# Optimization experiments

Hardware: AMD Instinct MI355X
Metric: run time of the kernel (lower is better)

## Reference

```python
import math
import jax, jax.numpy as jnp
import numpy as np

LN_EPS = 1e-5
SIG_DOMAIN = 5.0


def _layer_norm(x, gamma, beta):
    mu = jnp.mean(x, axis=-1, keepdims=True)
    var = jnp.var(x, axis=-1, keepdims=True)
    return (x - mu) / jnp.sqrt(var + LN_EPS) * gamma + beta


def setup_inputs() -> dict:
    key = jax.random.key(0)
    k0, k1, k2, k3 = jax.random.split(key, 4)
    B, H, S, D = 4, 16, 1024, 256   # batch, c_heads, seq, input_dim
    A, O = 128, 256                 # attention_dim, output_dim
    x = jax.random.normal(k0, (B, H, S, D), dtype=jnp.float32)
    # torch.rand -> uniform [0,1)
    W_query = jax.random.uniform(k1, (H, A, D), dtype=jnp.float32)
    W_key = jax.random.uniform(k2, (H, A, D), dtype=jnp.float32)
    W_value = jax.random.uniform(k3, (H, O, D), dtype=jnp.float32)
    gamma = jnp.ones((D,), dtype=jnp.float32)
    beta = jnp.zeros((D,), dtype=jnp.float32)
    return {"x": x, "W_query": W_query, "W_key": W_key, "W_value": W_value,
            "gamma": gamma, "beta": beta}


def reference(x, W_query, W_key, W_value, gamma, beta):
    scale = math.sqrt(x.shape[-1])  # sqrt(input_dim)
    xn = _layer_norm(x, gamma, beta)                       # [B,H,S,D]
    q = jnp.einsum('bhsd,had->bhsa', xn, W_query)          # [B,H,S,A]
    k = jnp.einsum('bhsd,had->bhsa', xn, W_key)            # [B,H,S,A]
    v = jnp.einsum('bhsd,hod->bhso', xn, W_value)          # [B,H,S,O]
    scores = jnp.einsum('bhsa,bhta->bhst', q, k) / scale   # [B,H,S,S]
    # overtaking-sigmoid-tuned normalization
    s_max = jnp.max(scores, axis=-1, keepdims=True)
    s_min = jnp.min(scores, axis=-1, keepdims=True)
    s_norm = (scores - s_min) / (s_max - s_min)
    softmax_sel = 1.0 - jax.nn.sigmoid(
        (1.0 - jnp.max(s_norm, axis=-1, keepdims=True)) * 2.0 * SIG_DOMAIN + SIG_DOMAIN)
    sigmoid_sel = 1.0 - softmax_sel
    weights = (softmax_sel * jax.nn.softmax(s_norm, axis=-1)
               + sigmoid_sel * jax.nn.sigmoid(s_norm * 2.0 * SIG_DOMAIN - SIG_DOMAIN))
    return jnp.einsum('bhst,bhto->bhso', weights, v)       # [B,H,S,O]
```

## Files before the change

kernel.cpp:

```cpp
#include <hip/hip_runtime.h>

typedef __attribute__((ext_vector_type(8))) short bf16x8;
typedef __attribute__((ext_vector_type(8))) _Float16 h16x8;
typedef __attribute__((ext_vector_type(4))) float f32x4;
typedef __attribute__((ext_vector_type(4))) unsigned short us4;
typedef unsigned short u16;

#define MFMA16 __builtin_amdgcn_mfma_f32_16x16x32_bf16

__device__ __forceinline__ u16 f2bf(float f) {
  union { float f; unsigned u; } v; v.f = f;
  unsigned r = v.u + 0x7FFFu + ((v.u >> 16) & 1u);
  return (u16)(r >> 16);
}

__global__ __launch_bounds__(256) void ln_kernel(const float* __restrict__ x,
    const float* __restrict__ gamma, const float* __restrict__ beta,
    u16* __restrict__ xn)
{
  int row = blockIdx.x * 4 + (threadIdx.x >> 6);
  int lane = threadIdx.x & 63;
  const float* xr = x + (size_t)row * 256;
  f32x4 v = *(const f32x4*)(xr + lane * 4);
  float s  = v[0] + v[1] + v[2] + v[3];
  float s2 = v[0]*v[0] + v[1]*v[1] + v[2]*v[2] + v[3]*v[3];
  #pragma unroll
  for (int off = 1; off < 64; off <<= 1) {
    s  += __shfl_xor(s, off);
    s2 += __shfl_xor(s2, off);
  }
  float mu   = s * (1.0f / 256.0f);
  float var  = s2 * (1.0f / 256.0f) - mu * mu;
  float rstd = rsqrtf(var + 1e-5f);
  f32x4 g  = *(const f32x4*)(gamma + lane * 4);
  f32x4 bb = *(const f32x4*)(beta  + lane * 4);
  us4 o;
  #pragma unroll
  for (int j = 0; j < 4; j++) o[j] = f2bf((v[j] - mu) * rstd * g[j] + bb[j]);
  *(us4*)(xn + (size_t)row * 256 + lane * 4) = o;
}

__global__ __launch_bounds__(256) void cvt_kernel(const float* __restrict__ in,
    u16* __restrict__ out, int n4)
{
  int i = blockIdx.x * 256 + threadIdx.x;
  if (i >= n4) return;
  f32x4 v = *(const f32x4*)(in + (size_t)i * 4);
  us4 o;
  #pragma unroll
  for (int j = 0; j < 4; j++) o[j] = f2bf(v[j]);
  *(us4*)(out + (size_t)i * 4) = o;
}

__global__ __launch_bounds__(256) void gemm128(const u16* __restrict__ Ag,
    const u16* __restrict__ Bg, u16* __restrict__ Cg,
    int M, int N, int aHead, int bHead)
{
  constexpr int K = 256;
  __shared__ u16 As[128][128];
  __shared__ u16 Bs[128][128];
  int bh = blockIdx.z;
  int m0 = blockIdx.x * 128, n0 = blockIdx.y * 128;
  const u16* Ab = Ag + (size_t)(aHead ? (bh & 15) : bh) * M * K + (size_t)m0 * K;
  const u16* Bb = Bg + (size_t)(bHead ? (bh & 15) : bh) * N * K + (size_t)n0 * K;
  int tid = threadIdx.x, lane = tid & 63, w = tid >> 6;
  int wm = w >> 1, wn = w & 1;
  int lr = lane & 15, g = lane >> 4;

  f32x4 acc[4][4] = {};
  for (int kc = 0; kc < 2; kc++) {
    if (kc) __syncthreads();
    #pragma unroll
    for (int i = 0; i < 8; i++) {
      int c = tid + 256 * i;
      int r = c >> 4, ch = c & 15;
      int sw = (ch ^ (r & 7)) * 8;
      *(bf16x8*)&As[r][sw] = *(const bf16x8*)(Ab + (size_t)r * K + kc * 128 + ch * 8);
      *(bf16x8*)&Bs[r][sw] = *(const bf16x8*)(Bb + (size_t)r * K + kc * 128 + ch * 8);
    }
    __syncthreads();
    #pragma unroll
    for (int ks = 0; ks < 4; ks++) {
      bf16x8 af[4], bfr[4];
      #pragma unroll
      for (int mf = 0; mf < 4; mf++) {
        int r = wm * 64 + mf * 16 + lr;
        af[mf] = *(const bf16x8*)&As[r][((ks * 4 + g) ^ (r & 7)) * 8];
      }
      #pragma unroll
      for (int nf = 0; nf < 4; nf++) {
        int r = wn * 64 + nf * 16 + lr;
        bfr[nf] = *(const bf16x8*)&Bs[r][((ks * 4 + g) ^ (r & 7)) * 8];
      }
      #pragma unroll
      for (int mf = 0; mf < 4; mf++)
        #pragma unroll
        for (int nf = 0; nf < 4; nf++)
          acc[mf][nf] = MFMA16(af[mf], bfr[nf], acc[mf][nf], 0, 0, 0);
    }
  }
  u16* Cb = Cg + (size_t)bh * M * N;
  #pragma unroll
  for (int mf = 0; mf < 4; mf++)
    #pragma unroll
    for (int nf = 0; nf < 4; nf++)
      #pragma unroll
      for (int i = 0; i < 4; i++) {
        int row = m0 + wm * 64 + mf * 16 + g * 4 + i;
        int col = n0 + wn * 64 + nf * 16 + lr;
        Cb[(size_t)row * N + col] = f2bf(acc[mf][nf][i]);
      }
}

__global__ __launch_bounds__(256) void score_kernel(
    const u16* __restrict__ Qg, const u16* __restrict__ Kg,
    _Float16* __restrict__ Sg, float2* __restrict__ rp, int bh0)
{
  constexpr int S = 1024, AD = 128;
  __shared__ u16 Qs[128][128];
  __shared__ u16 Ks[128][128];
  int bid = blockIdx.x;
  int hl = ((bid >> 6) << 3) | (bid & 7);
  int rb = (bid >> 3) & 7;
  int bh = bh0 + hl;
  int m0 = rb * 128;
  int tid = threadIdx.x, lane = tid & 63, w = tid >> 6;
  int lr = lane & 15, g = lane >> 4;
  const u16* Qb = Qg + ((size_t)bh * S + m0) * AD;
  const u16* Kb = Kg + (size_t)bh * S * AD;

  #pragma unroll
  for (int i = 0; i < 8; i++) {
    int c = tid + 256 * i;
    int r = c >> 4, ch = c & 15;
    *(bf16x8*)&Qs[r][(ch ^ (r & 7)) * 8] = *(const bf16x8*)(Qb + (size_t)r * AD + ch * 8);
  }
  __syncthreads();

  bf16x8 af[2][4];
  #pragma unroll
  for (int mf = 0; mf < 2; mf++)
    #pragma unroll
    for (int ks = 0; ks < 4; ks++) {
      int r = w * 32 + mf * 16 + lr;
      af[mf][ks] = *(const bf16x8*)&Qs[r][((ks * 4 + g) ^ (r & 7)) * 8];
    }

  float rmin[2][4], rmax[2][4];
  #pragma unroll
  for (int mf = 0; mf < 2; mf++)
    #pragma unroll
    for (int i = 0; i < 4; i++) { rmin[mf][i] = 3.0e38f; rmax[mf][i] = -3.0e38f; }

  _Float16* Sb = Sg + (size_t)hl * S * S;
  for (int nc = 0; nc < 8; nc++) {
    __syncthreads();
    const u16* Kp = Kb + (size_t)nc * 128 * AD;
    #pragma unroll
    for (int i = 0; i < 8; i++) {
      int c = tid + 256 * i;
      int r = c >> 4, ch = c & 15;
      *(bf16x8*)&Ks[r][(ch ^ (r & 7)) * 8] = *(const bf16x8*)(Kp + (size_t)r * AD + ch * 8);
    }
    __syncthreads();

    f32x4 acc[2][8] = {};
    #pragma unroll
    for (int ks = 0; ks < 4; ks++) {
      bf16x8 bk[8];
      #pragma unroll
      for (int nf = 0; nf < 8; nf++) {
        int r = nf * 16 + lr;
        bk[nf] = *(const bf16x8*)&Ks[r][((ks * 4 + g) ^ (r & 7)) * 8];
      }
      #pragma unroll
      for (int mf = 0; mf < 2; mf++)
        #pragma unroll
        for (int nf = 0; nf < 8; nf++)
          acc[mf][nf] = MFMA16(af[mf][ks], bk[nf], acc[mf][nf], 0, 0, 0);
    }
    #pragma unroll
    for (int mf = 0; mf < 2; mf++)
      #pragma unroll
      for (int nf = 0; nf < 8; nf++)
        #pragma unroll
        for (int i = 0; i < 4; i++) {
          int row = m0 + w * 32 + mf * 16 + g * 4 + i;
          int col = nc * 128 + nf * 16 + lr;
          Sb[(size_t)row * S + col] = (_Float16)acc[mf][nf][i];
          rmin[mf][i] = fminf(rmin[mf][i], acc[mf][nf][i]);
          rmax[mf][i] = fmaxf(rmax[mf][i], acc[mf][nf][i]);
        }
  }
  #pragma unroll
  for (int off = 1; off < 16; off <<= 1)
    #pragma unroll
    for (int mf = 0; mf < 2; mf++)
      #pragma unroll
      for (int i = 0; i < 4; i++) {
        rmin[mf][i] = fminf(rmin[mf][i], __shfl_xor(rmin[mf][i], off));
        rmax[mf][i] = fmaxf(rmax[mf][i], __shfl_xor(rmax[mf][i], off));
      }
  if (lr == 0) {
    #pragma unroll
    for (int mf = 0; mf < 2; mf++)
      #pragma unroll
      for (int i = 0; i < 4; i++) {
        int row = m0 + w * 32 + mf * 16 + g * 4 + i;
        float inv = 1.0f / (rmax[mf][i] - rmin[mf][i]);
        rp[(size_t)bh * S + row] = make_float2(10.0f * inv, fmaf(-10.0f * rmin[mf][i], inv, -5.0f));
      }
  }
}

__global__ __launch_bounds__(256) void pv_kernel(
    const _Float16* __restrict__ Sg, const float2* __restrict__ rpG,
    const u16* __restrict__ VTg, float* __restrict__ Out, int bh0)
{
  constexpr int S = 1024, OD = 256;
  __shared__ u16 Bs[2][256 * 34];
  int bid = blockIdx.x;
  int hl = ((bid >> 6) << 3) | (bid & 7);
  int rb = (bid >> 3) & 7;
  int bh = bh0 + hl;
  int m0 = rb * 128;
  int tid = threadIdx.x, lane = tid & 63, w = tid >> 6;
  int lr = lane & 15, g = lane >> 4;
  const _Float16* Sb = Sg + (size_t)hl * S * S;
  const u16* Vb = VTg + (size_t)bh * OD * S;

  float am[2], bm[2];
  const _Float16* Srow[2];
  #pragma unroll
  for (int mf = 0; mf < 2; mf++) {
    int row = m0 + w * 32 + mf * 16 + lr;
    float2 p = rpG[(size_t)bh * S + row];
    am[mf] = -p.x * 1.44269504f;
    bm[mf] = -p.y * 1.44269504f;
    Srow[mf] = Sb + (size_t)row * S + g * 8;
  }

  f32x4 acc[2][16] = {};

  bf16x8 pre[4];
  h16x8 svc[2], svn[2];
  #pragma unroll
  for (int i = 0; i < 4; i++) pre[i] = *(const bf16x8*)(Vb + (size_t)tid * S + i * 8);
  #pragma unroll
  for (int i = 0; i < 4; i++) *(bf16x8*)&Bs[0][tid * 34 + i * 8] = pre[i];
  #pragma unroll
  for (int mf = 0; mf < 2; mf++) svc[mf] = *(const h16x8*)(Srow[mf]);
  __syncthreads();

  for (int kt = 0; kt < 32; kt++) {
    int cur = kt & 1;
    if (kt < 31) {
      #pragma unroll
      for (int i = 0; i < 4; i++)
        pre[i] = *(const bf16x8*)(Vb + (size_t)tid * S + (kt + 1) * 32 + i * 8);
      #pragma unroll
      for (int mf = 0; mf < 2; mf++) svn[mf] = *(const h16x8*)(Srow[mf] + (kt + 1) * 32);
    }
    bf16x8 pa[2];
    #pragma unroll
    for (int mf = 0; mf < 2; mf++)
      #pragma unroll
      for (int q = 0; q < 8; q++) {
        float e = exp2f(fmaf((float)svc[mf][q], am[mf], bm[mf]));
        pa[mf][q] = (short)f2bf(__builtin_amdgcn_rcpf(1.0f + e));
      }
    __builtin_amdgcn_s_setprio(1);
    #pragma unroll
    for (int nf = 0; nf < 16; nf++) {
      bf16x8 bv = *(const bf16x8*)&Bs[cur][(nf * 16 + lr) * 34 + g * 8];
      acc[0][nf] = MFMA16(pa[0], bv, acc[0][nf], 0, 0, 0);
      acc[1][nf] = MFMA16(pa[1], bv, acc[1][nf], 0, 0, 0);
    }
    __builtin_amdgcn_s_setprio(0);
    if (kt < 31) {
      #pragma unroll
      for (int i = 0; i < 4; i++) *(bf16x8*)&Bs[cur ^ 1][tid * 34 + i * 8] = pre[i];
      svc[0] = svn[0]; svc[1] = svn[1];
    }
    __syncthreads();
  }

  const float c2 = 0.9933071490757153f;
  float* Ob = Out + ((size_t)bh * S + m0 + w * 32) * OD;
  #pragma unroll
  for (int mf = 0; mf < 2; mf++)
    #pragma unroll
    for (int nf = 0; nf < 16; nf++)
      #pragma unroll
      for (int i = 0; i < 4; i++) {
        int row = mf * 16 + g * 4 + i;
        int col = nf * 16 + lr;
        Ob[(size_t)row * OD + col] = c2 * acc[mf][nf][i];
      }
}

extern "C" void kernel_launch(void* const* d_in, const int* in_sizes, int n_in,
                              void* d_out, int out_size, void* d_ws, size_t ws_size,
                              hipStream_t stream) {
  const float* x     = (const float*)d_in[0];
  const float* Wq    = (const float*)d_in[1];
  const float* Wk    = (const float*)d_in[2];
  const float* Wv    = (const float*)d_in[3];
  const float* gamma = (const float*)d_in[4];
  const float* beta  = (const float*)d_in[5];
  float* out = (float*)d_out;

  constexpr int B = 4, H = 16, S = 1024, D = 256, A = 128, O = 256;
  constexpr int BH = B * H;

  char* p = (char*)d_ws;
  size_t off = 0;
  auto take = [&](size_t n) { off = (off + 255) & ~(size_t)255; char* q = p + off; off += n; return q; };

  u16*    xn  = (u16*)take((size_t)BH * S * D * 2);
  u16*    qb  = (u16*)take((size_t)BH * S * A * 2);
  u16*    kb  = (u16*)take((size_t)BH * S * A * 2);
  u16*    vtb = (u16*)take((size_t)BH * O * S * 2);
  u16*    wqb = (u16*)take((size_t)H * A * D * 2);
  u16*    wkb = (u16*)take((size_t)H * A * D * 2);
  u16*    wvb = (u16*)take((size_t)H * O * D * 2);
  float2* rp  = (float2*)take((size_t)BH * S * 8);

  int grp = 1;
  for (; grp < 8; grp <<= 1) {
    size_t need = ((off + 255) & ~(size_t)255) + (size_t)(BH / grp) * S * S * 2;
    if (need <= ws_size) break;
  }
  int hp = BH / grp;
  _Float16* sG = (_Float16*)take((size_t)hp * S * S * 2);

  ln_kernel<<<BH * S / 4, 256, 0, stream>>>(x, gamma, beta, xn);

  cvt_kernel<<<(H * A * D / 4 + 255) / 256, 256, 0, stream>>>(Wq, wqb, H * A * D / 4);
  cvt_kernel<<<(H * A * D / 4 + 255) / 256, 256, 0, stream>>>(Wk, wkb, H * A * D / 4);
  cvt_kernel<<<(H * O * D / 4 + 255) / 256, 256, 0, stream>>>(Wv, wvb, H * O * D / 4);

  gemm128<<<dim3(S / 128, A / 128, BH), 256, 0, stream>>>(xn, wqb, qb, S, A, 0, 1);
  gemm128<<<dim3(S / 128, A / 128, BH), 256, 0, stream>>>(xn, wkb, kb, S, A, 0, 1);
  gemm128<<<dim3(O / 128, S / 128, BH), 256, 0, stream>>>(wvb, xn, vtb, O, S, 1, 0);

  for (int gi = 0; gi < grp; gi++) {
    int bh0 = gi * hp;
    score_kernel<<<hp * 8, 256, 0, stream>>>(qb, kb, sG, rp, bh0);
    pv_kernel<<<hp * 8, 256, 0, stream>>>(sG, rp, vtb, out, bh0);
  }
}
```

Baseline: 176.6 us.

## Fuse Q/K projections, prefetch K tiles via registers, use fp16 PV MFMA

Q and K weights are packed into one interleaved matrix so a single GEMM produces a combined QK buffer, replacing two projection launches. The score kernel now loads the next K tile into registers while computing on the current one, replacing the synchronous per-chunk reload with register-staged double buffering. V is emitted in fp16 and the PV matmul uses f16 MFMA, with probabilities packed through cvt_pkrtz and a raw exp2 builtin instead of software bf16 rounding. Using fp16 for V changes precision and carries overflow risk if V values exceed the fp16 range.

```diff
diff --git a/kernel.cpp b/kernel.cpp
--- a/kernel.cpp
+++ b/kernel.cpp
@@ -2,16 +2,27 @@
 
 typedef __attribute__((ext_vector_type(8))) short bf16x8;
 typedef __attribute__((ext_vector_type(8))) _Float16 h16x8;
+typedef __attribute__((ext_vector_type(2))) _Float16 h16x2;
+typedef __attribute__((ext_vector_type(2))) __fp16 fp16x2;
 typedef __attribute__((ext_vector_type(4))) float f32x4;
 typedef __attribute__((ext_vector_type(4))) unsigned short us4;
 typedef unsigned short u16;
 
-#define MFMA16 __builtin_amdgcn_mfma_f32_16x16x32_bf16
+#define MFMA16  __builtin_amdgcn_mfma_f32_16x16x32_bf16
+#define MFMA16H __builtin_amdgcn_mfma_f32_16x16x32_f16
 
 __device__ __forceinline__ u16 f2bf(float f) {
   union { float f; unsigned u; } v; v.f = f;
   unsigned r = v.u + 0x7FFFu + ((v.u >> 16) & 1u);
   return (u16)(r >> 16);
+}
+
+__device__ __forceinline__ float ex2(float x) {
+#if __has_builtin(__builtin_amdgcn_exp2f)
+  return __builtin_amdgcn_exp2f(x);
+#else
+  return exp2f(x);
+#endif
 }
 
 __global__ __launch_bounds__(256) void ln_kernel(const float* __restrict__ x,
@@ -52,9 +63,23 @@
   *(us4*)(out + (size_t)i * 4) = o;
 }
 
+__global__ __launch_bounds__(256) void cvt_qk(const float* __restrict__ in,
+    u16* __restrict__ out, int half)
+{
+  int i = blockIdx.x * 256 + threadIdx.x;
+  int e4 = i * 4;
+  int h = e4 >> 15;
+  int rem = e4 & 32767;
+  f32x4 v = *(const f32x4*)(in + e4);
+  us4 o;
+  #pragma unroll
+  for (int j = 0; j < 4; j++) o[j] = f2bf(v[j]);
+  *(us4*)(out + (size_t)h * 65536 + half * 32768 + rem) = o;
+}
+
 __global__ __launch_bounds__(256) void gemm128(const u16* __restrict__ Ag,
     const u16* __restrict__ Bg, u16* __restrict__ Cg,
-    int M, int N, int aHead, int bHead)
+    int M, int N, int aHead, int bHead, int outHalf)
 {
   constexpr int K = 256;
   __shared__ u16 As[128][128];
@@ -108,15 +133,17 @@
       for (int i = 0; i < 4; i++) {
         int row = m0 + wm * 64 + mf * 16 + g * 4 + i;
         int col = n0 + wn * 64 + nf * 16 + lr;
-        Cb[(size_t)row * N + col] = f2bf(acc[mf][nf][i]);
+        u16 ev;
+        if (outHalf) { _Float16 hv = (_Float16)acc[mf][nf][i]; ev = *(u16*)&hv; }
+        else ev = f2bf(acc[mf][nf][i]);
+        Cb[(size_t)row * N + col] = ev;
       }
 }
 
 __global__ __launch_bounds__(256) void score_kernel(
-    const u16* __restrict__ Qg, const u16* __restrict__ Kg,
-    _Float16* __restrict__ Sg, float2* __restrict__ rp, int bh0)
-{
-  constexpr int S = 1024, AD = 128;
+    const u16* __restrict__ QKg, _Float16* __restrict__ Sg, float2* __restrict__ rp, int bh0)
+{
+  constexpr int S = 1024, LD = 256;
   __shared__ u16 Qs[128][128];
   __shared__ u16 Ks[128][128];
   int bid = blockIdx.x;
@@ -126,24 +153,25 @@
   int m0 = rb * 128;
   int tid = threadIdx.x, lane = tid & 63, w = tid >> 6;
   int lr = lane & 15, g = lane >> 4;
-  const u16* Qb = Qg + ((size_t)bh * S + m0) * AD;
-  const u16* Kb = Kg + (size_t)bh * S * AD;
+  const u16* Qb = QKg + ((size_t)bh * S + m0) * LD;
+  const u16* Kb = QKg + (size_t)bh * S * LD + 128;
 
   #pragma unroll
   for (int i = 0; i < 8; i++) {
     int c = tid + 256 * i;
     int r = c >> 4, ch = c & 15;
-    *(bf16x8*)&Qs[r][(ch ^ (r & 7)) * 8] = *(const bf16x8*)(Qb + (size_t)r * AD + ch * 8);
+    *(bf16x8*)&Qs[r][(ch ^ (r & 7)) * 8] = *(const bf16x8*)(Qb + (size_t)r * LD + ch * 8);
+    *(bf16x8*)&Ks[r][(ch ^ (r & 7)) * 8] = *(const bf16x8*)(Kb + (size_t)r * LD + ch * 8);
   }
   __syncthreads();
 
-  bf16x8 af[2][4];
+  bf16x8 aq[2][4];
   #pragma unroll
   for (int mf = 0; mf < 2; mf++)
     #pragma unroll
     for (int ks = 0; ks < 4; ks++) {
       int r = w * 32 + mf * 16 + lr;
-      af[mf][ks] = *(const bf16x8*)&Qs[r][((ks * 4 + g) ^ (r & 7)) * 8];
+      aq[mf][ks] = *(const bf16x8*)&Qs[r][((ks * 4 + g) ^ (r & 7)) * 8];
     }
 
   float rmin[2][4], rmax[2][4];
@@ -154,16 +182,15 @@
 
   _Float16* Sb = Sg + (size_t)hl * S * S;
   for (int nc = 0; nc < 8; nc++) {
-    __syncthreads();
-    const u16* Kp = Kb + (size_t)nc * 128 * AD;
-    #pragma unroll
-    for (int i = 0; i < 8; i++) {
-      int c = tid + 256 * i;
-      int r = c >> 4, ch = c & 15;
-      *(bf16x8*)&Ks[r][(ch ^ (r & 7)) * 8] = *(const bf16x8*)(Kp + (size_t)r * AD + ch * 8);
-    }
-    __syncthreads();
-
+    bf16x8 kreg[8];
+    if (nc < 7) {
+      #pragma unroll
+      for (int i = 0; i < 8; i++) {
+        int c = tid + 256 * i;
+        int r = c >> 4, ch = c & 15;
+        kreg[i] = *(const bf16x8*)(Kb + (size_t)(128 * (nc + 1) + r) * LD + ch * 8);
+      }
+    }
     f32x4 acc[2][8] = {};
     #pragma unroll
     for (int ks = 0; ks < 4; ks++) {
@@ -177,7 +204,7 @@
       for (int mf = 0; mf < 2; mf++)
         #pragma unroll
         for (int nf = 0; nf < 8; nf++)
-          acc[mf][nf] = MFMA16(af[mf][ks], bk[nf], acc[mf][nf], 0, 0, 0);
+          acc[mf][nf] = MFMA16(aq[mf][ks], bk[nf], acc[mf][nf], 0, 0, 0);
     }
     #pragma unroll
     for (int mf = 0; mf < 2; mf++)
@@ -191,6 +218,16 @@
           rmin[mf][i] = fminf(rmin[mf][i], acc[mf][nf][i]);
           rmax[mf][i] = fmaxf(rmax[mf][i], acc[mf][nf][i]);
         }
+    __syncthreads();
+    if (nc < 7) {
+      #pragma unroll
+      for (int i = 0; i < 8; i++) {
+        int c = tid + 256 * i;
+        int r = c >> 4, ch = c & 15;
+        *(bf16x8*)&Ks[r][(ch ^ (r & 7)) * 8] = kreg[i];
+      }
+    }
+    __syncthreads();
   }
   #pragma unroll
   for (int off = 1; off < 16; off <<= 1)
@@ -248,8 +285,8 @@
   for (int i = 0; i < 4; i++) pre[i] = *(const bf16x8*)(Vb + (size_t)tid * S + i * 8);
   #pragma unroll
   for (int i = 0; i < 4; i++) *(bf16x8*)&Bs[0][tid * 34 + i * 8] = pre[i];
-  #pragma unroll
-  for (int mf = 0; mf < 2; mf++) svc[mf] = *(const h16x8*)(Srow[mf]);
+  svc[0] = *(const h16x8*)(Srow[0]);
+  svc[1] = *(const h16x8*)(Srow[1]);
   __syncthreads();
 
   for (int kt = 0; kt < 32; kt++) {
@@ -258,23 +295,28 @@
       #pragma unroll
       for (int i = 0; i < 4; i++)
         pre[i] = *(const bf16x8*)(Vb + (size_t)tid * S + (kt + 1) * 32 + i * 8);
-      #pragma unroll
-      for (int mf = 0; mf < 2; mf++) svn[mf] = *(const h16x8*)(Srow[mf] + (kt + 1) * 32);
-    }
-    bf16x8 pa[2];
-    #pragma unroll
-    for (int mf = 0; mf < 2; mf++)
-      #pragma unroll
-      for (int q = 0; q < 8; q++) {
-        float e = exp2f(fmaf((float)svc[mf][q], am[mf], bm[mf]));
-        pa[mf][q] = (short)f2bf(__builtin_amdgcn_rcpf(1.0f + e));
-      }
+      svn[0] = *(const h16x8*)(Srow[0] + (kt + 1) * 32);
+      svn[1] = *(const h16x8*)(Srow[1] + (kt + 1) * 32);
+    }
+    h16x8 pa[2];
+    #pragma unroll
+    for (int mf = 0; mf < 2; mf++) {
+      h16x2* pw = (h16x2*)&pa[mf];
+      #pragma unroll
+      for (int q = 0; q < 4; q++) {
+        float e0 = ex2(fmaf((float)svc[mf][2*q],     am[mf], bm[mf]));
+        float e1 = ex2(fmaf((float)svc[mf][2*q + 1], am[mf], bm[mf]));
+        fp16x2 pk = __builtin_amdgcn_cvt_pkrtz(__builtin_amdgcn_rcpf(1.0f + e0),
+                                               __builtin_amdgcn_rcpf(1.0f + e1));
+        pw[q] = __builtin_bit_cast(h16x2, pk);
+      }
+    }
     __builtin_amdgcn_s_setprio(1);
     #pragma unroll
     for (int nf = 0; nf < 16; nf++) {
-      bf16x8 bv = *(const bf16x8*)&Bs[cur][(nf * 16 + lr) * 34 + g * 8];
-      acc[0][nf] = MFMA16(pa[0], bv, acc[0][nf], 0, 0, 0);
-      acc[1][nf] = MFMA16(pa[1], bv, acc[1][nf], 0, 0, 0);
+      h16x8 bv = *(const h16x8*)&Bs[cur][(nf * 16 + lr) * 34 + g * 8];
+      acc[0][nf] = MFMA16H(pa[0], bv, acc[0][nf], 0, 0, 0);
+      acc[1][nf] = MFMA16H(pa[1], bv, acc[1][nf], 0, 0, 0);
     }
     __builtin_amdgcn_s_setprio(0);
     if (kt < 31) {
@@ -317,14 +359,12 @@
   size_t off = 0;
   auto take = [&](size_t n) { off = (off + 255) & ~(size_t)255; char* q = p + off; off += n; return q; };
 
-  u16*    xn  = (u16*)take((size_t)BH * S * D * 2);
-  u16*    qb  = (u16*)take((size_t)BH * S * A * 2);
-  u16*    kb  = (u16*)take((size_t)BH * S * A * 2);
-  u16*    vtb = (u16*)take((size_t)BH * O * S * 2);
-  u16*    wqb = (u16*)take((size_t)H * A * D * 2);
-  u16*    wkb = (u16*)take((size_t)H * A * D * 2);
-  u16*    wvb = (u16*)take((size_t)H * O * D * 2);
-  float2* rp  = (float2*)take((size_t)BH * S * 8);
+  u16*    xn   = (u16*)take((size_t)BH * S * D * 2);
+  u16*    qkb  = (u16*)take((size_t)BH * S * 256 * 2);
+  u16*    vtb  = (u16*)take((size_t)BH * O * S * 2);
+  u16*    wqkb = (u16*)take((size_t)H * 256 * D * 2);
+  u16*    wvb  = (u16*)take((size_t)H * O * D * 2);
+  float2* rp   = (float2*)take((size_t)BH * S * 8);
 
   int grp = 1;
   for (; grp < 8; grp <<= 1) {
@@ -336,17 +376,16 @@
 
   ln_kernel<<<BH * S / 4, 256, 0, stream>>>(x, gamma, beta, xn);
 
-  cvt_kernel<<<(H * A * D / 4 + 255) / 256, 256, 0, stream>>>(Wq, wqb, H * A * D / 4);
-  cvt_kernel<<<(H * A * D / 4 + 255) / 256, 256, 0, stream>>>(Wk, wkb, H * A * D / 4);
+  cvt_qk<<<(H * A * D / 4) / 256, 256, 0, stream>>>(Wq, wqkb, 0);
+  cvt_qk<<<(H * A * D / 4) / 256, 256, 0, stream>>>(Wk, wqkb, 1);
   cvt_kernel<<<(H * O * D / 4 + 255) / 256, 256, 0, stream>>>(Wv, wvb, H * O * D / 4);
 
-  gemm128<<<dim3(S / 128, A / 128, BH), 256, 0, stream>>>(xn, wqb, qb, S, A, 0, 1);
-  gemm128<<<dim3(S / 128, A / 128, BH), 256, 0, stream>>>(xn, wkb, kb, S, A, 0, 1);
-  gemm128<<<dim3(O / 128, S / 128, BH), 256, 0, stream>>>(wvb, xn, vtb, O, S, 1, 0);
+  gemm128<<<dim3(S / 128, 256 / 128, BH), 256, 0, stream>>>(xn, wqkb, qkb, S, 256, 0, 1, 0);
+  gemm128<<<dim3(O / 128, S / 128, BH), 256, 0, stream>>>(wvb, xn, vtb, O, S, 1, 0, 1);
 
   for (int gi = 0; gi < grp; gi++) {
     int bh0 = gi * hp;
-    score_kernel<<<hp * 8, 256, 0, stream>>>(qb, kb, sG, rp, bh0);
+    score_kernel<<<hp * 8, 256, 0, stream>>>(qkb, sG, rp, bh0);
     pv_kernel<<<hp * 8, 256, 0, stream>>>(sG, rp, vtb, out, bh0);
   }
 }
```

New measurement: 175.2 us. Within noise of the previous version (-0.8%).
